# Performance work log

Measured on AMD Instinct MI355X. Metric: run time of the kernel, lower is better.

Reference implementation:

```python
import jax, jax.numpy as jnp
import numpy as np


def setup_inputs() -> dict:
    key = jax.random.key(0)
    ks = jax.random.split(key, 7)
    B, C, W, H = 4, 256, 64, 64
    C8 = C // 8
    return {
        "x": jax.random.normal(ks[0], (B, C, W, H), dtype=jnp.float32),
        "Wq": jax.random.normal(ks[1], (C8, C), dtype=jnp.float32) * 0.05,
        "bq": jax.random.normal(ks[2], (C8,), dtype=jnp.float32) * 0.05,
        "Wk": jax.random.normal(ks[3], (C8, C), dtype=jnp.float32) * 0.05,
        "bk": jax.random.normal(ks[4], (C8,), dtype=jnp.float32) * 0.05,
        "Wv": jax.random.normal(ks[5], (C, C), dtype=jnp.float32) * 0.05,
        "bv": jax.random.normal(ks[6], (C,), dtype=jnp.float32) * 0.05,
    }


def reference(x, Wq, bq, Wk, bk, Wv, bv):
    B, C, W, H = x.shape
    N = W * H
    xf = x.reshape(B, C, N)  # flatten spatial dims
    # 1x1 convs == per-position linear projections
    q = jnp.einsum('oc,bcn->bno', Wq, xf) + bq            # (B, N, C/8)
    k = jnp.einsum('oc,bcn->bon', Wk, xf) + bk[None, :, None]  # (B, C/8, N)
    # attention scores (B, N, N); original applies softmax over dim=1
    attn = jax.nn.softmax(jnp.einsum('bno,bom->bnm', q, k), axis=1)
    v = jnp.einsum('oc,bcn->bno', Wv, xf) + bv            # (B, N, C)
    out = jnp.einsum('bnm,bmc->bnc', attn, v)             # (B, N, C)
    # faithful to original: raw view of (B, N, C) as (B, C, W, H)
    return out.reshape(B, C, W, H)
```

## Files before the change

### kernel.cpp

```cpp
#include <hip/hip_runtime.h>
#include <math.h>

#define NB 4
#define CC 256
#define CO 32
#define NN 4096
#define MU 320
#define LOG2E 1.44269504088896f

typedef __attribute__((ext_vector_type(4))) float f4;
typedef __attribute__((ext_vector_type(8))) short s8;
typedef __attribute__((ext_vector_type(8))) unsigned short us8;
typedef __attribute__((ext_vector_type(2))) unsigned int u2;
typedef __attribute__((ext_vector_type(4))) unsigned int u4i;

__device__ __forceinline__ unsigned short f2bf(float f) {
    unsigned int u = __float_as_uint(f);
    u = (u + 0x7FFFu + ((u >> 16) & 1u)) >> 16;
    return (unsigned short)u;
}
__device__ __forceinline__ unsigned int cvtpk(float lo, float hi) {
    unsigned int r;
    asm("v_cvt_pk_bf16_f32 %0, %1, %2" : "=v"(r) : "v"(lo), "v"(hi));
    return r;
}
__device__ __forceinline__ int swz128(int row, int colByte) {
    return row * 128 + (colByte ^ ((row & 7) << 4));
}
#define LDS_BARRIER() asm volatile("s_waitcnt lgkmcnt(0)\n\ts_barrier" ::: "memory")

union s8u4 { s8 s; u4i u; };

__global__ __launch_bounds__(256) void prepw_kernel(
    const float* __restrict__ Wq, const float* __restrict__ bq,
    const float* __restrict__ Wk, const float* __restrict__ bk,
    const float* __restrict__ Wv, const float* __restrict__ bv,
    unsigned short* __restrict__ Wb, float* __restrict__ fb)
{
    const int t = threadIdx.x;
    #pragma unroll
    for (int i = 0; i < 4; ++i) {
        const int e = blockIdx.x * 1024 + i * 256 + t;
        const int u = e >> 8, c = e & 255;
        float val = (u < 32) ? Wq[u * 256 + c]
                  : (u < 64) ? Wk[(u - 32) * 256 + c]
                             : Wv[(u - 64) * 256 + c];
        Wb[e] = f2bf(val);
    }
    if (blockIdx.x == 0) {
        for (int u = t; u < MU; u += 256)
            fb[u] = (u < 32) ? bq[u] : (u < 64) ? bk[u - 32] : bv[u - 64];
    }
}

__global__ __launch_bounds__(256) void projf_kernel(
    const float* __restrict__ x, const unsigned short* __restrict__ Wb,
    const float* __restrict__ fb,
    unsigned short* __restrict__ qb, unsigned short* __restrict__ kb,
    unsigned short* __restrict__ vtb)
{
    __shared__ float xl[32][260];

    const int t   = threadIdx.x;
    const int b   = blockIdx.x >> 7;
    const int nbl = blockIdx.x & 127;
    const int n0  = nbl * 32;

    {
        const int nl = t & 7;
        const int c8 = t >> 3;
        #pragma unroll
        for (int pass = 0; pass < 8; ++pass) {
            const int c = c8 + pass * 32;
            f4 xv = *reinterpret_cast<const f4*>(x + ((size_t)(b * CC + c)) * NN + n0 + nl * 4);
            #pragma unroll
            for (int j = 0; j < 4; ++j) xl[nl * 4 + j][c] = xv[j];
        }
    }
    __syncthreads();

    const int w    = t >> 6;
    const int l    = t & 63;
    const int l15  = l & 15;
    const int g4   = l >> 4;
    const int nw   = w & 1;
    const int uw   = w >> 1;
    const int nloc = nw * 16 + l15;
    const int n    = n0 + nloc;

    s8 bfr[8];
    #pragma unroll
    for (int kk = 0; kk < 8; ++kk) {
        f4 a  = *reinterpret_cast<const f4*>(&xl[nloc][kk * 32 + g4 * 8]);
        f4 c2 = *reinterpret_cast<const f4*>(&xl[nloc][kk * 32 + g4 * 8 + 4]);
        s8u4 tmp;
        tmp.u = (u4i){ cvtpk(a[0], a[1]), cvtpk(a[2], a[3]),
                       cvtpk(c2[0], c2[1]), cvtpk(c2[2], c2[3]) };
        bfr[kk] = tmp.s;
    }

    const f4 z = {0.f, 0.f, 0.f, 0.f};
    unsigned short* qrow = qb + ((size_t)(b * NN + n)) * CO;
    unsigned short* krow = kb + ((size_t)(b * NN + n)) * CO;

    #pragma unroll
    for (int i = 0; i < 10; ++i) {
        const int u0 = (uw * 10 + i) * 16;
        f4 acc = z;
        #pragma unroll
        for (int kk = 0; kk < 8; ++kk) {
            s8 af = *reinterpret_cast<const s8*>(Wb + (size_t)(u0 + l15) * CC + kk * 32 + g4 * 8);
            acc = __builtin_amdgcn_mfma_f32_16x16x32_bf16(af, bfr[kk], acc, 0, 0, 0);
        }
        f4 bias4 = *reinterpret_cast<const f4*>(fb + u0 + g4 * 4);
        if (u0 < 32) {
            u2 pw = { cvtpk((acc[0] + bias4[0]) * LOG2E, (acc[1] + bias4[1]) * LOG2E),
                      cvtpk((acc[2] + bias4[2]) * LOG2E, (acc[3] + bias4[3]) * LOG2E) };
            *reinterpret_cast<u2*>(qrow + u0 + g4 * 4) = pw;
        } else if (u0 < 64) {
            u2 pw = { cvtpk(acc[0] + bias4[0], acc[1] + bias4[1]),
                      cvtpk(acc[2] + bias4[2], acc[3] + bias4[3]) };
            *reinterpret_cast<u2*>(krow + (u0 - 32) + g4 * 4) = pw;
        } else {
            const int cbase = u0 - 64 + g4 * 4;
            #pragma unroll
            for (int r = 0; r < 4; ++r)
                vtb[((size_t)(b * CC + cbase + r)) * NN + n] = f2bf(acc[r] + bias4[r]);
        }
    }
}

__global__ __launch_bounds__(256) void colstats_kernel(
    const unsigned short* __restrict__ qb, const unsigned short* __restrict__ kb,
    const unsigned short* __restrict__ vtb, unsigned short* __restrict__ vfr)
{
    __shared__ float red[4][16];
    __shared__ float civl[16];

    const int t   = threadIdx.x;
    const int b   = blockIdx.x >> 8;
    const int mb  = blockIdx.x & 255;
    const int l   = t & 63;
    const int w   = t >> 6;
    const int l15 = l & 15;
    const int g4  = l >> 4;
    const int m   = mb * 16 + l15;

    const unsigned short* qbB = qb + (size_t)b * NN * CO;
    s8 kfrag = *reinterpret_cast<const s8*>(kb + ((size_t)b * NN + m) * CO + g4 * 8);

    const f4 z = {0.f, 0.f, 0.f, 0.f};
    float ssum = 0.f;

    const int nbeg = w * 1024, nend = nbeg + 1024;
    for (int n0 = nbeg; n0 < nend; n0 += 32) {
        s8 a0 = *reinterpret_cast<const s8*>(qbB + (size_t)(n0 + l15) * CO + g4 * 8);
        s8 a1 = *reinterpret_cast<const s8*>(qbB + (size_t)(n0 + 16 + l15) * CO + g4 * 8);
        f4 d0 = __builtin_amdgcn_mfma_f32_16x16x32_bf16(a0, kfrag, z, 0, 0, 0);
        f4 d1 = __builtin_amdgcn_mfma_f32_16x16x32_bf16(a1, kfrag, z, 0, 0, 0);
        #pragma unroll
        for (int r = 0; r < 4; ++r) ssum += exp2f(d0[r]) + exp2f(d1[r]);
    }

    ssum += __shfl_xor(ssum, 16);
    ssum += __shfl_xor(ssum, 32);
    if (l < 16) red[w][l15] = ssum;
    __syncthreads();
    if (w == 0 && l < 16)
        civl[l15] = 1.0f / (red[0][l15] + red[1][l15] + red[2][l15] + red[3][l15]);
    __syncthreads();

    const int mt   = mb >> 2;
    const int ksl  = (mb >> 1) & 1;
    const int g4b  = (mb & 1) * 2;
    const int cg   = t >> 4;
    const int l15v = t & 15;
    const unsigned short* vp = vtb + ((size_t)(b * CC + t)) * NN + mb * 16;
    unsigned short* dst = vfr + (size_t)b * 1048576
                        + (((mt * 16 + cg) * 2 + ksl) << 9)
                        + (g4b * 16 + l15v) * 8;
    #pragma unroll
    for (int i = 0; i < 2; ++i) {
        us8 vv = *reinterpret_cast<const us8*>(vp + i * 8);
        u4i o;
        #pragma unroll
        for (int e2 = 0; e2 < 4; ++e2) {
            float f0 = __uint_as_float((unsigned int)vv[2 * e2]     << 16) * civl[i * 8 + 2 * e2];
            float f1 = __uint_as_float((unsigned int)vv[2 * e2 + 1] << 16) * civl[i * 8 + 2 * e2 + 1];
            o[e2] = cvtpk(f0, f1);
        }
        *reinterpret_cast<u4i*>(dst + i * 128) = o;
    }
}

__global__ __launch_bounds__(512, 4) void attn_kernel(
    const unsigned short* __restrict__ qb, const unsigned short* __restrict__ kb,
    const unsigned short* __restrict__ vfr, float* __restrict__ out)
{
    __shared__ __align__(16) char plds[2][32 * 128];

    const int t   = threadIdx.x;
    const int w   = t >> 6;
    const int l   = t & 63;
    const int l15 = l & 15;
    const int g4  = l >> 4;
    const int bid  = (blockIdx.x & 7) * 64 + (blockIdx.x >> 3);
    const int b    = bid >> 7;
    const int nblk = bid & 127;
    const int n0   = nblk * 32;
    const int ng   = w >> 2;
    const int mq   = w & 3;

    const unsigned short* qbB = qb + (size_t)b * NN * CO;
    const unsigned short* kbB = kb + (size_t)b * NN * CO;

    s8 qfrag = *reinterpret_cast<const s8*>(qbB + (size_t)(n0 + ng * 16 + l15) * CO + g4 * 8);

    const int pwo  = swz128(ng * 16 + l15, mq * 32 + g4 * 8);
    const int pr00 = swz128(l15,      g4 * 16);
    const int pr01 = swz128(l15,      64 + g4 * 16);
    const int pr10 = swz128(16 + l15, g4 * 16);
    const int pr11 = swz128(16 + l15, 64 + g4 * 16);

    const unsigned short* kp = kbB + (size_t)(mq * 16 + l15) * CO + g4 * 8;
    const unsigned short* vp = vfr + (size_t)b * 1048576 + w * 2048 + l * 8;

    s8 kreg;
    s8 v0, v1, v2, v3;
    const f4 z = {0.f, 0.f, 0.f, 0.f};
    f4 acc00 = z, acc01 = z, acc10 = z, acc11 = z;

#define LOADK() do { kreg = *reinterpret_cast<const s8*>(kp); kp += 2048; } while (0)
#define LOADV() do { \
        v0 = *reinterpret_cast<const s8*>(vp); \
        v1 = *reinterpret_cast<const s8*>(vp + 512); \
        v2 = *reinterpret_cast<const s8*>(vp + 1024); \
        v3 = *reinterpret_cast<const s8*>(vp + 1536); \
        vp += 16384; \
    } while (0)

#define STAGE(BUF, KR) do { \
        f4 d = __builtin_amdgcn_mfma_f32_16x16x32_bf16(KR, qfrag, z, 0, 0, 0); \
        u2 pw = { cvtpk(exp2f(d[0]), exp2f(d[1])), cvtpk(exp2f(d[2]), exp2f(d[3])) }; \
        *reinterpret_cast<u2*>(plds[BUF] + pwo) = pw; \
    } while (0)

#define PVSTEP(BUF) do { \
        s8 pa00 = *reinterpret_cast<const s8*>(plds[BUF] + pr00); \
        s8 pa01 = *reinterpret_cast<const s8*>(plds[BUF] + pr01); \
        s8 pa10 = *reinterpret_cast<const s8*>(plds[BUF] + pr10); \
        s8 pa11 = *reinterpret_cast<const s8*>(plds[BUF] + pr11); \
        __builtin_amdgcn_s_setprio(1); \
        acc00 = __builtin_amdgcn_mfma_f32_16x16x32_bf16(pa00, v0, acc00, 0, 0, 0); \
        acc01 = __builtin_amdgcn_mfma_f32_16x16x32_bf16(pa00, v2, acc01, 0, 0, 0); \
        acc10 = __builtin_amdgcn_mfma_f32_16x16x32_bf16(pa10, v0, acc10, 0, 0, 0); \
        acc11 = __builtin_amdgcn_mfma_f32_16x16x32_bf16(pa10, v2, acc11, 0, 0, 0); \
        acc00 = __builtin_amdgcn_mfma_f32_16x16x32_bf16(pa01, v1, acc00, 0, 0, 0); \
        acc01 = __builtin_amdgcn_mfma_f32_16x16x32_bf16(pa01, v3, acc01, 0, 0, 0); \
        acc10 = __builtin_amdgcn_mfma_f32_16x16x32_bf16(pa11, v1, acc10, 0, 0, 0); \
        acc11 = __builtin_amdgcn_mfma_f32_16x16x32_bf16(pa11, v3, acc11, 0, 0, 0); \
        __builtin_amdgcn_s_setprio(0); \
    } while (0)

    s8 k0 = *reinterpret_cast<const s8*>(kp); kp += 2048;
    LOADK();
    LOADV();
    STAGE(0, k0);
    LDS_BARRIER();

    for (int i = 0; i < 64; i += 2) {
        STAGE(1, kreg);
        if (i < 62) LOADK();
        PVSTEP(0);
        if (i < 63) LOADV();
        LDS_BARRIER();

        if (i + 1 < 63) STAGE(0, kreg);
        if (i + 1 < 62) LOADK();
        PVSTEP(1);
        if (i + 1 < 63) LOADV();
        LDS_BARRIER();
    }

#undef LOADK
#undef LOADV
#undef STAGE
#undef PVSTEP

    float* ob = out + (size_t)b * NN * CC;
    const int cw = w * 32 + l15;
    #pragma unroll
    for (int r = 0; r < 4; ++r) {
        const size_t row0 = (size_t)(n0 + g4 * 4 + r) * CC;
        const size_t row1 = (size_t)(n0 + 16 + g4 * 4 + r) * CC;
        ob[row0 + cw]      = acc00[r];
        ob[row0 + cw + 16] = acc01[r];
        ob[row1 + cw]      = acc10[r];
        ob[row1 + cw + 16] = acc11[r];
    }
}

extern "C" void kernel_launch(void* const* d_in, const int* in_sizes, int n_in,
                              void* d_out, int out_size, void* d_ws, size_t ws_size,
                              hipStream_t stream)
{
    const float* x  = (const float*)d_in[0];
    const float* Wq = (const float*)d_in[1];
    const float* bq = (const float*)d_in[2];
    const float* Wk = (const float*)d_in[3];
    const float* bk = (const float*)d_in[4];
    const float* Wv = (const float*)d_in[5];
    const float* bv = (const float*)d_in[6];
    float* out = (float*)d_out;

    unsigned short* qb  = (unsigned short*)d_ws;
    unsigned short* kb  = qb  + (size_t)NB * NN * CO;
    unsigned short* vtb = kb  + (size_t)NB * NN * CO;
    unsigned short* vfr = vtb + (size_t)NB * CC * NN;
    unsigned short* Wb  = vfr + (size_t)NB * CC * NN;
    float*          fb  = (float*)(Wb + (size_t)MU * CC);

    prepw_kernel<<<dim3(80), dim3(256), 0, stream>>>(Wq, bq, Wk, bk, Wv, bv, Wb, fb);
    projf_kernel<<<dim3(512), dim3(256), 0, stream>>>(x, Wb, fb, qb, kb, vtb);
    colstats_kernel<<<dim3(1024), dim3(256), 0, stream>>>(qb, kb, vtb, vfr);
    attn_kernel<<<dim3(512), dim3(512), 0, stream>>>(qb, kb, vfr, out);
}
```

Before: 112.0 us.

## Deepen attention pipeline to four LDS P buffers with double-buffered K/V registers

Expands the probability LDS staging from two to four buffers and keeps two K/V register sets in flight. Each barrier interval now stages and consumes two score tiles instead of one, which halves the number of LDS barriers per loop. It also lengthens the prefetch distance for K and V global loads. The loop-tail guards were removed, so the final iterations issue loads past the last tile and do unused work. The extra live V and K registers raise register pressure under the 512x4 launch bound and could spill or lower occupancy.

```diff
diff --git a/kernel.cpp b/kernel.cpp
--- a/kernel.cpp
+++ b/kernel.cpp
@@ -197,7 +197,7 @@
     const unsigned short* __restrict__ qb, const unsigned short* __restrict__ kb,
     const unsigned short* __restrict__ vfr, float* __restrict__ out)
 {
-    __shared__ __align__(16) char plds[2][32 * 128];
+    __shared__ __align__(16) char plds[4][32 * 128];
 
     const int t   = threadIdx.x;
     const int w   = t >> 6;
@@ -225,17 +225,26 @@
     const unsigned short* kp = kbB + (size_t)(mq * 16 + l15) * CO + g4 * 8;
     const unsigned short* vp = vfr + (size_t)b * 1048576 + w * 2048 + l * 8;
 
-    s8 kreg;
-    s8 v0, v1, v2, v3;
     const f4 z = {0.f, 0.f, 0.f, 0.f};
     f4 acc00 = z, acc01 = z, acc10 = z, acc11 = z;
 
-#define LOADK() do { kreg = *reinterpret_cast<const s8*>(kp); kp += 2048; } while (0)
-#define LOADV() do { \
-        v0 = *reinterpret_cast<const s8*>(vp); \
-        v1 = *reinterpret_cast<const s8*>(vp + 512); \
-        v2 = *reinterpret_cast<const s8*>(vp + 1024); \
-        v3 = *reinterpret_cast<const s8*>(vp + 1536); \
+    s8 kA, kB, kC, kD;
+    s8 vA0, vA1, vA2, vA3;
+    s8 vB0, vB1, vB2, vB3;
+
+#define LOADK(KR) do { KR = *reinterpret_cast<const s8*>(kp); kp += 2048; } while (0)
+#define LOADVA() do { \
+        vA0 = *reinterpret_cast<const s8*>(vp); \
+        vA1 = *reinterpret_cast<const s8*>(vp + 512); \
+        vA2 = *reinterpret_cast<const s8*>(vp + 1024); \
+        vA3 = *reinterpret_cast<const s8*>(vp + 1536); \
+        vp += 16384; \
+    } while (0)
+#define LOADVB() do { \
+        vB0 = *reinterpret_cast<const s8*>(vp); \
+        vB1 = *reinterpret_cast<const s8*>(vp + 512); \
+        vB2 = *reinterpret_cast<const s8*>(vp + 1024); \
+        vB3 = *reinterpret_cast<const s8*>(vp + 1536); \
         vp += 16384; \
     } while (0)
 
@@ -245,45 +254,54 @@
         *reinterpret_cast<u2*>(plds[BUF] + pwo) = pw; \
     } while (0)
 
-#define PVSTEP(BUF) do { \
+#define PVSTEP(BUF, V0, V1, V2, V3) do { \
         s8 pa00 = *reinterpret_cast<const s8*>(plds[BUF] + pr00); \
         s8 pa01 = *reinterpret_cast<const s8*>(plds[BUF] + pr01); \
         s8 pa10 = *reinterpret_cast<const s8*>(plds[BUF] + pr10); \
         s8 pa11 = *reinterpret_cast<const s8*>(plds[BUF] + pr11); \
         __builtin_amdgcn_s_setprio(1); \
-        acc00 = __builtin_amdgcn_mfma_f32_16x16x32_bf16(pa00, v0, acc00, 0, 0, 0); \
-        acc01 = __builtin_amdgcn_mfma_f32_16x16x32_bf16(pa00, v2, acc01, 0, 0, 0); \
-        acc10 = __builtin_amdgcn_mfma_f32_16x16x32_bf16(pa10, v0, acc10, 0, 0, 0); \
-        acc11 = __builtin_amdgcn_mfma_f32_16x16x32_bf16(pa10, v2, acc11, 0, 0, 0); \
-        acc00 = __builtin_amdgcn_mfma_f32_16x16x32_bf16(pa01, v1, acc00, 0, 0, 0); \
-        acc01 = __builtin_amdgcn_mfma_f32_16x16x32_bf16(pa01, v3, acc01, 0, 0, 0); \
-        acc10 = __builtin_amdgcn_mfma_f32_16x16x32_bf16(pa11, v1, acc10, 0, 0, 0); \
-        acc11 = __builtin_amdgcn_mfma_f32_16x16x32_bf16(pa11, v3, acc11, 0, 0, 0); \
+        acc00 = __builtin_amdgcn_mfma_f32_16x16x32_bf16(pa00, V0, acc00, 0, 0, 0); \
+        acc01 = __builtin_amdgcn_mfma_f32_16x16x32_bf16(pa00, V2, acc01, 0, 0, 0); \
+        acc10 = __builtin_amdgcn_mfma_f32_16x16x32_bf16(pa10, V0, acc10, 0, 0, 0); \
+        acc11 = __builtin_amdgcn_mfma_f32_16x16x32_bf16(pa10, V2, acc11, 0, 0, 0); \
+        acc00 = __builtin_amdgcn_mfma_f32_16x16x32_bf16(pa01, V1, acc00, 0, 0, 0); \
+        acc01 = __builtin_amdgcn_mfma_f32_16x16x32_bf16(pa01, V3, acc01, 0, 0, 0); \
+        acc10 = __builtin_amdgcn_mfma_f32_16x16x32_bf16(pa11, V1, acc10, 0, 0, 0); \
+        acc11 = __builtin_amdgcn_mfma_f32_16x16x32_bf16(pa11, V3, acc11, 0, 0, 0); \
         __builtin_amdgcn_s_setprio(0); \
     } while (0)
 
-    s8 k0 = *reinterpret_cast<const s8*>(kp); kp += 2048;
-    LOADK();
-    LOADV();
+    s8 k0, k1;
+    LOADK(k0); LOADK(k1);
+    LOADK(kA); LOADK(kB);
+    LOADK(kC); LOADK(kD);
+    LOADVA();
+    LOADVB();
     STAGE(0, k0);
+    STAGE(1, k1);
     LDS_BARRIER();
 
-    for (int i = 0; i < 64; i += 2) {
-        STAGE(1, kreg);
-        if (i < 62) LOADK();
-        PVSTEP(0);
-        if (i < 63) LOADV();
+    for (int i = 0; i < 64; i += 4) {
+        STAGE(2, kA); LOADK(kA);
+        STAGE(3, kB); LOADK(kB);
+        PVSTEP(0, vA0, vA1, vA2, vA3);
+        LOADVA();
+        PVSTEP(1, vB0, vB1, vB2, vB3);
+        LOADVB();
         LDS_BARRIER();
 
-        if (i + 1 < 63) STAGE(0, kreg);
-        if (i + 1 < 62) LOADK();
-        PVSTEP(1);
-        if (i + 1 < 63) LOADV();
+        STAGE(0, kC); LOADK(kC);
+        STAGE(1, kD); LOADK(kD);
+        PVSTEP(2, vA0, vA1, vA2, vA3);
+        LOADVA();
+        PVSTEP(3, vB0, vB1, vB2, vB3);
+        LOADVB();
         LDS_BARRIER();
     }
 
 #undef LOADK
-#undef LOADV
+#undef LOADVA
+#undef LOADVB
 #undef STAGE
 #undef PVSTEP
 
```

Result: no change. 112.2 us, median of 2 (+0.2%).
